# Performance work log

Hardware: AMD Instinct MI355X
Metric: run time of the kernel (lower is better)

The kernel has to match this reference:

```python
import jax, jax.numpy as jnp
import numpy as np

EMBED_DIM = 768
NUM_HEADS = 12
SEGMENT_LENGTHS = (2048, 4096, 8192)
DILATION_RATES = (1, 2, 4)
LN_EPS = 1e-5


def setup_inputs() -> dict:
    rng = jax.random.key(0)
    ks = jax.random.split(rng, 6)
    B, S, E = 2, 8192, EMBED_DIM
    xavier = (2.0 / (E + E)) ** 0.5  # xavier_normal std for square fan-in/out
    return {
        "query": jax.random.normal(ks[0], (B, S, E), jnp.float32),
        "key": jax.random.normal(ks[1], (B, S, E), jnp.float32),
        "value": jax.random.normal(ks[2], (B, S, E), jnp.float32),
        "qkv_w": jax.random.normal(ks[3], (3 * E, E), jnp.float32) * xavier,
        "qkv_b": jnp.zeros((3 * E,), jnp.float32),
        "ln_w": jnp.ones((E,), jnp.float32),
        "ln_b": jnp.zeros((E,), jnp.float32),
        "out_w": jax.random.normal(ks[4], (E, E), jnp.float32) * xavier,
        "out_b": jnp.zeros((E,), jnp.float32),
    }


def _dilated_attention(q, k, v):
    # q,k,v: [b, n, h, d].  Heads are partitioned across the
    # (segment_length, dilation_rate) groups; within each group the sequence
    # is split into segments of length s and subsampled with stride r at
    # offset (i % r); plain softmax attention runs inside each dilated segment.
    b, n, h, d = q.shape
    G = len(SEGMENT_LENGTHS)
    g = h // G
    scale = 1.0 / np.sqrt(d)
    out = jnp.zeros_like(q)
    for i, (s, r) in enumerate(zip(SEGMENT_LENGTHS, DILATION_RATES)):
        off = i % r
        h0, h1 = i * g, (i + 1) * g
        m = n // s
        def seg(x):
            # [b, n, g, d] -> [b, m, s/r, g, d]
            return x[:, :, h0:h1].reshape(b, m, s, g, d)[:, :, off::r]
        qi, ki, vi = seg(q), seg(k), seg(v)
        scores = jnp.einsum("bmqgd,bmkgd->bmgqk", qi, ki) * scale
        p = jax.nn.softmax(scores, axis=-1)
        xi = jnp.einsum("bmgqk,bmkgd->bmqgd", p, vi)
        seg_out = jnp.zeros((b, m, s, g, d), q.dtype).at[:, :, off::r].set(xi)
        out = out.at[:, :, h0:h1].set(seg_out.reshape(b, n, g, d))
    return out / G


def reference(query, key, value, qkv_w, qkv_b, ln_w, ln_b, out_w, out_b):
    B, S, E = query.shape
    H = NUM_HEADS
    d = E // H
    # fused QKV projection (cross-attention path of the fused projection)
    q = (query @ qkv_w[:E].T + qkv_b[:E]).reshape(B, S, H, d)
    k = (key @ qkv_w[E:2 * E].T + qkv_b[E:2 * E]).reshape(B, S, H, d)
    v = (value @ qkv_w[2 * E:].T + qkv_b[2 * E:]).reshape(B, S, H, d)
    x = _dilated_attention(q, k, v).reshape(B, S, E)
    # MAGNETO layer norm before output projection
    mu = jnp.mean(x, axis=-1, keepdims=True)
    var = jnp.mean(jnp.square(x - mu), axis=-1, keepdims=True)
    x = (x - mu) * jax.lax.rsqrt(var + LN_EPS) * ln_w + ln_b
    return x @ out_w.T + out_b
```

## Files before the change

### kernel.cpp

```cpp
#include <hip/hip_runtime.h>
#include <hip/hip_bf16.h>
#include <math.h>

typedef __bf16 bf16_t;
typedef __bf16 bf16x8 __attribute__((ext_vector_type(8)));
typedef __bf16 bf16x4 __attribute__((ext_vector_type(4)));
typedef float f32x4 __attribute__((ext_vector_type(4)));

__device__ __forceinline__ void async_ld16(const void* g, void* l) {
  __builtin_amdgcn_global_load_lds(
      (const __attribute__((address_space(1))) unsigned int*)g,
      (__attribute__((address_space(3))) unsigned int*)l, 16, 0, 0);
}

#define BATCH 2
#define SEQ   8192
#define EMB   768
#define NHEAD 12
#define HD    64
#define TOK   (BATCH*SEQ)
#define GATH_PER_B 57344

__device__ __forceinline__ int headoff(int h) {
  int g = h >> 2;
  int base = (g == 0) ? 0 : ((g == 1) ? 32768 : 49152);
  return base + (h & 3) * (8192 >> g);
}

__global__ void k_cast(const float* __restrict__ in, bf16_t* __restrict__ out, int n) {
  int i = (blockIdx.x * blockDim.x + threadIdx.x) * 8;
  if (i < n) {
    float4 a = *(const float4*)(in + i);
    float4 b = *(const float4*)(in + i + 4);
    __attribute__((aligned(16))) bf16_t o[8] = {
        (bf16_t)a.x, (bf16_t)a.y, (bf16_t)a.z, (bf16_t)a.w,
        (bf16_t)b.x, (bf16_t)b.y, (bf16_t)b.z, (bf16_t)b.w};
    *(uint4*)(out + i) = *(uint4*)o;
  }
}

__global__ __launch_bounds__(256, 2)
void k_gemm_qkv(const bf16_t* __restrict__ qb, const bf16_t* __restrict__ kb,
                const bf16_t* __restrict__ vb, const bf16_t* __restrict__ wqkv,
                const float* __restrict__ qkv_bias,
                bf16_t* __restrict__ Qg, bf16_t* __restrict__ Kg, bf16_t* __restrict__ Vb) {
  const int N = 768, K = 768;
  int z = blockIdx.z;
  const bf16_t* A = (z == 0) ? qb : (z == 1) ? kb : vb;
  const bf16_t* W = wqkv + (size_t)z * N * K;
  const float* bias = qkv_bias + z * N;

  __shared__ bf16_t As[128][32];
  __shared__ bf16_t Bs[128][32];

  int tid = threadIdx.x;
  int wave = tid >> 6, lane = tid & 63;
  int q = lane >> 4, c = lane & 15;
  int wm = (wave & 1) * 64, wn = (wave >> 1) * 64;
  int m0 = blockIdx.y * 128, n0 = blockIdx.x * 128;

  f32x4 acc[4][4];
#pragma unroll
  for (int i = 0; i < 4; i++)
#pragma unroll
    for (int j = 0; j < 4; j++) acc[i][j] = (f32x4){0.f, 0.f, 0.f, 0.f};

  for (int k0 = 0; k0 < K; k0 += 32) {
#pragma unroll
    for (int it = 0; it < 2; ++it) {
      int ch = tid + it * 256;
      int row = ch >> 2, kb8 = (ch & 3) << 3;
      async_ld16(A + (size_t)(m0 + row) * K + k0 + kb8, &As[row][kb8]);
      async_ld16(W + (size_t)(n0 + row) * K + k0 + kb8, &Bs[row][kb8]);
    }
    __syncthreads();
    bf16x8 af[4], bfr[4];
#pragma unroll
    for (int mi = 0; mi < 4; mi++) af[mi] = *(const bf16x8*)&As[wm + mi * 16 + c][q * 8];
#pragma unroll
    for (int nj = 0; nj < 4; nj++) bfr[nj] = *(const bf16x8*)&Bs[wn + nj * 16 + c][q * 8];
#pragma unroll
    for (int mi = 0; mi < 4; mi++)
#pragma unroll
      for (int nj = 0; nj < 4; nj++)
        acc[mi][nj] = __builtin_amdgcn_mfma_f32_16x16x32_bf16(af[mi], bfr[nj], acc[mi][nj], 0, 0, 0);
    __syncthreads();
  }

  if (z == 2) {
#pragma unroll
    for (int mi = 0; mi < 4; mi++)
#pragma unroll
      for (int nj = 0; nj < 4; nj++)
#pragma unroll
        for (int rg = 0; rg < 4; rg++) {
          int row = m0 + wm + mi * 16 + q * 4 + rg;
          int col = n0 + wn + nj * 16 + c;
          Vb[(size_t)row * N + col] = (bf16_t)(acc[mi][nj][rg] + bias[col]);
        }
  } else {
    bf16_t* dst = (z == 0) ? Qg : Kg;
    float qscale = (z == 0) ? 0.125f : 1.0f;
#pragma unroll
    for (int mi = 0; mi < 4; mi++)
#pragma unroll
      for (int nj = 0; nj < 4; nj++) {
        int e = n0 + wn + nj * 16 + c;
        int h = e >> 6, dim = e & 63, g2 = h >> 2;
        int rm1 = (1 << g2) - 1, sh = 11 + g2;
        int smask = (2048 << g2) - 1;
        int ho = headoff(h);
#pragma unroll
        for (int rg = 0; rg < 4; rg++) {
          int row = m0 + wm + mi * 16 + q * 4 + rg;
          float v = (acc[mi][nj][rg] + bias[e]) * qscale;
          int bb = row >> 13, p = row & 8191;
          int t = (p & smask) - g2;
          if (t >= 0 && (t & rm1) == 0) {
            int jj = (p >> sh) * 2048 + (t >> g2);
            dst[(size_t)(bb * GATH_PER_B + ho + jj) * HD + dim] = (bf16_t)v;
          }
        }
      }
  }
}

__global__ __launch_bounds__(256, 2)
void k_gemm_out(const bf16_t* __restrict__ A, const bf16_t* __restrict__ W,
                const float* __restrict__ bias, float* __restrict__ C) {
  const int N = 768, K = 768;
  __shared__ bf16_t As[128][32];
  __shared__ bf16_t Bs[128][32];

  int tid = threadIdx.x;
  int wave = tid >> 6, lane = tid & 63;
  int q = lane >> 4, c = lane & 15;
  int wm = (wave & 1) * 64, wn = (wave >> 1) * 64;
  int m0 = blockIdx.y * 128, n0 = blockIdx.x * 128;

  f32x4 acc[4][4];
#pragma unroll
  for (int i = 0; i < 4; i++)
#pragma unroll
    for (int j = 0; j < 4; j++) acc[i][j] = (f32x4){0.f, 0.f, 0.f, 0.f};

  for (int k0 = 0; k0 < K; k0 += 32) {
#pragma unroll
    for (int it = 0; it < 2; ++it) {
      int ch = tid + it * 256;
      int row = ch >> 2, kb8 = (ch & 3) << 3;
      async_ld16(A + (size_t)(m0 + row) * K + k0 + kb8, &As[row][kb8]);
      async_ld16(W + (size_t)(n0 + row) * K + k0 + kb8, &Bs[row][kb8]);
    }
    __syncthreads();
    bf16x8 af[4], bfr[4];
#pragma unroll
    for (int mi = 0; mi < 4; mi++) af[mi] = *(const bf16x8*)&As[wm + mi * 16 + c][q * 8];
#pragma unroll
    for (int nj = 0; nj < 4; nj++) bfr[nj] = *(const bf16x8*)&Bs[wn + nj * 16 + c][q * 8];
#pragma unroll
    for (int mi = 0; mi < 4; mi++)
#pragma unroll
      for (int nj = 0; nj < 4; nj++)
        acc[mi][nj] = __builtin_amdgcn_mfma_f32_16x16x32_bf16(af[mi], bfr[nj], acc[mi][nj], 0, 0, 0);
    __syncthreads();
  }
#pragma unroll
  for (int mi = 0; mi < 4; mi++)
#pragma unroll
    for (int nj = 0; nj < 4; nj++)
#pragma unroll
      for (int rg = 0; rg < 4; rg++) {
        int row = m0 + wm + mi * 16 + q * 4 + rg;
        int col = n0 + wn + nj * 16 + c;
        C[(size_t)row * N + col] = acc[mi][nj][rg] + bias[col];
      }
}

__global__ __launch_bounds__(256)
void k_gather_v(const bf16_t* __restrict__ Vb, bf16_t* __restrict__ Vt) {
  int h = blockIdx.y, b = blockIdx.z;
  int g = h >> 2;
  int L = 8192 >> g;
  int jj0 = blockIdx.x * 64;
  if (jj0 >= L) return;
  int s = 2048 << g;
  int hb = b * GATH_PER_B + headoff(h);
  int tid = threadIdx.x;

  __shared__ bf16_t tile[64][72];

#pragma unroll
  for (int it = 0; it < 2; ++it) {
    int ch = tid + it * 256;
    int rowl = ch >> 3, db = (ch & 7) << 3;
    int jj = jj0 + rowl;
    int p = (jj >> 11) * s + g + ((jj & 2047) << g);
    *(uint4*)&tile[rowl][db] = *(const uint4*)(Vb + ((size_t)(b * SEQ + p)) * EMB + h * HD + db);
  }
  __syncthreads();
  int dim = tid >> 2, sub = tid & 3;
  __attribute__((aligned(16))) bf16_t tmp[16];
#pragma unroll
  for (int sl = 0; sl < 16; sl++) {
    int t = sub * 16 + sl;
    int pos = (t & 3) * 16 + (t >> 2);
    tmp[sl] = tile[pos][dim];
  }
  size_t vdst = ((size_t)hb) * HD + (size_t)dim * L + jj0 + sub * 16;
  *(uint4*)(Vt + vdst) = *(uint4*)&tmp[0];
  *(uint4*)(Vt + vdst + 8) = *(uint4*)&tmp[8];
}

__global__ __launch_bounds__(256, 3)
void k_attn(const bf16_t* __restrict__ Qg, const bf16_t* __restrict__ Kg,
            const bf16_t* __restrict__ Vt, bf16_t* __restrict__ xattn) {
  int u = blockIdx.x;
  int seg = u % 56, qt = u / 56;
  int b = seg / 28, t = seg % 28;
  int g, h, si;
  if (t < 16)      { g = 0; h = t >> 2;              si = t & 3; }
  else if (t < 24) { g = 1; h = 4 + ((t - 16) >> 1); si = (t - 16) & 1; }
  else             { g = 2; h = 8 + (t - 24);        si = 0; }
  int L = 8192 >> g, s = 2048 << g;
  int hb = b * GATH_PER_B + headoff(h);
  int jj0 = si * 2048 + qt * 128;
  int kvbase = si * 2048;

  __shared__ bf16_t Ps[128][64];
  __shared__ bf16_t Ks[128][64];
  __shared__ bf16_t Vs[64][128];

  int tid = threadIdx.x, wave = tid >> 6, lane = tid & 63;
  int q = lane >> 4, c = lane & 15;
  int cx = c & 7;
  int wm = wave * 32;

  bf16_t* Qs = &Ps[0][0];
#pragma unroll
  for (int it = 0; it < 4; ++it) {
    int ch = tid + it * 256;
    int row = ch >> 3, pc = ch & 7, lc = pc ^ (row & 7);
    async_ld16(Qg + ((size_t)(hb + jj0 + row)) * HD + lc * 8, Qs + ch * 8);
  }
  __syncthreads();
  bf16x8 aq[2][2];
#pragma unroll
  for (int mi = 0; mi < 2; mi++)
#pragma unroll
    for (int kq = 0; kq < 2; kq++) {
      int pch = (kq * 4 + q) ^ cx;
      aq[mi][kq] = *(const bf16x8*)(Qs + (size_t)(wm + mi * 16 + c) * HD + pch * 8);
    }

  float lrow[2][4];
  f32x4 O[2][4];
#pragma unroll
  for (int mi = 0; mi < 2; mi++)
#pragma unroll
    for (int rg = 0; rg < 4; rg++) lrow[mi][rg] = 0.f;
#pragma unroll
  for (int mi = 0; mi < 2; mi++)
#pragma unroll
    for (int vd = 0; vd < 4; vd++) O[mi][vd] = (f32x4){0.f, 0.f, 0.f, 0.f};

  for (int kt = 0; kt < 16; ++kt) {
    __syncthreads();
#pragma unroll
    for (int it = 0; it < 4; ++it) {
      int ch = tid + it * 256;
      int row = ch >> 3, pc = ch & 7, lc = pc ^ (row & 7);
      async_ld16(Kg + ((size_t)(hb + kvbase + kt * 128 + row)) * HD + lc * 8,
                 &Ks[0][0] + ch * 8);
    }
#pragma unroll
    for (int it = 0; it < 4; ++it) {
      int ch = tid + it * 256;
      int dim = ch >> 4, pc = ch & 15, lc = pc ^ (dim & 7);
      async_ld16(Vt + ((size_t)hb) * HD + (size_t)dim * L + kvbase + kt * 128 + lc * 8,
                 &Vs[0][0] + ch * 8);
    }
    __syncthreads();

    f32x4 Sv[2][8];
#pragma unroll
    for (int mi = 0; mi < 2; mi++)
#pragma unroll
      for (int nj = 0; nj < 8; nj++) Sv[mi][nj] = (f32x4){0.f, 0.f, 0.f, 0.f};
#pragma unroll
    for (int kq = 0; kq < 2; kq++) {
      int pch = (kq * 4 + q) ^ cx;
      bf16x8 bk[8];
#pragma unroll
      for (int nj = 0; nj < 8; nj++) bk[nj] = *(const bf16x8*)&Ks[nj * 16 + c][pch * 8];
#pragma unroll
      for (int mi = 0; mi < 2; mi++)
#pragma unroll
        for (int nj = 0; nj < 8; nj++)
          Sv[mi][nj] = __builtin_amdgcn_mfma_f32_16x16x32_bf16(aq[mi][kq], bk[nj], Sv[mi][nj], 0, 0, 0);
    }

#pragma unroll
    for (int half = 0; half < 2; ++half) {
#pragma unroll
      for (int mi = 0; mi < 2; mi++)
#pragma unroll
        for (int rg = 0; rg < 4; rg++) {
          bf16x4 p4;
          float rs = 0.f;
#pragma unroll
          for (int j = 0; j < 4; j++) {
            float p = __expf(Sv[mi][half * 4 + j][rg]);
            rs += p;
            p4[j] = (bf16_t)p;
          }
          lrow[mi][rg] += rs;
          int row = wm + mi * 16 + q * 4 + rg;
          int u8 = c ^ ((row & 7) << 1);
          *(bf16x4*)((char*)&Ps[row][0] + u8 * 8) = p4;
        }
#pragma unroll
      for (int kk2 = 0; kk2 < 2; ++kk2) {
        bf16x8 ap[2], bv[4];
#pragma unroll
        for (int mi = 0; mi < 2; mi++) {
          int u8 = (kk2 * 8 + q * 2) ^ (cx << 1);
          ap[mi] = *(const bf16x8*)((char*)&Ps[wm + mi * 16 + c][0] + u8 * 8);
        }
#pragma unroll
        for (int vd = 0; vd < 4; vd++) {
          int pch = (half * 8 + kk2 * 4 + q) ^ cx;
          bv[vd] = *(const bf16x8*)&Vs[vd * 16 + c][pch * 8];
        }
#pragma unroll
        for (int mi = 0; mi < 2; mi++)
#pragma unroll
          for (int vd = 0; vd < 4; vd++)
            O[mi][vd] = __builtin_amdgcn_mfma_f32_16x16x32_bf16(ap[mi], bv[vd], O[mi][vd], 0, 0, 0);
      }
    }
  }

  const float inv3 = 1.0f / 3.0f;
#pragma unroll
  for (int mi = 0; mi < 2; mi++)
#pragma unroll
    for (int rg = 0; rg < 4; rg++) {
      float l = lrow[mi][rg];
#pragma unroll
      for (int d = 1; d < 16; d <<= 1) l += __shfl_xor(l, d, 64);
      float invl = inv3 / l;
      int jj = jj0 + wm + mi * 16 + q * 4 + rg;
      int p = si * s + g + ((jj & 2047) << g);
      size_t base = ((size_t)(b * SEQ + p)) * EMB + h * HD;
#pragma unroll
      for (int vd = 0; vd < 4; vd++)
        xattn[base + vd * 16 + c] = (bf16_t)(O[mi][vd][rg] * invl);
    }
}

__global__ __launch_bounds__(256)
void k_ln(const bf16_t* __restrict__ x, const float* __restrict__ lnw,
          const float* __restrict__ lnb, bf16_t* __restrict__ y) {
  int wave = threadIdx.x >> 6, lane = threadIdx.x & 63;
  int row = blockIdx.x * 4 + wave;
  const bf16_t* xr = x + (size_t)row * EMB + lane * 12;
  bf16x4 v4[3];
#pragma unroll
  for (int j = 0; j < 3; j++) v4[j] = *(const bf16x4*)(xr + j * 4);
  float v[12], s = 0.f, s2 = 0.f;
#pragma unroll
  for (int j = 0; j < 12; j++) {
    v[j] = (float)v4[j >> 2][j & 3];
    s += v[j];
    s2 += v[j] * v[j];
  }
#pragma unroll
  for (int d = 1; d < 64; d <<= 1) { s += __shfl_xor(s, d, 64); s2 += __shfl_xor(s2, d, 64); }
  float mu = s * (1.f / 768.f);
  float var = s2 * (1.f / 768.f) - mu * mu;
  float rstd = rsqrtf(var + 1e-5f);
  const float4* wr = (const float4*)(lnw + lane * 12);
  const float4* br = (const float4*)(lnb + lane * 12);
  bf16_t* yr = y + (size_t)row * EMB + lane * 12;
#pragma unroll
  for (int j = 0; j < 3; j++) {
    float4 w = wr[j], bb = br[j];
    bf16x4 o;
    o[0] = (bf16_t)((v[j * 4 + 0] - mu) * rstd * w.x + bb.x);
    o[1] = (bf16_t)((v[j * 4 + 1] - mu) * rstd * w.y + bb.y);
    o[2] = (bf16_t)((v[j * 4 + 2] - mu) * rstd * w.z + bb.z);
    o[3] = (bf16_t)((v[j * 4 + 3] - mu) * rstd * w.w + bb.w);
    *(bf16x4*)(yr + j * 4) = o;
  }
}

extern "C" void kernel_launch(void* const* d_in, const int* in_sizes, int n_in,
                              void* d_out, int out_size, void* d_ws, size_t ws_size,
                              hipStream_t stream) {
  const float* query = (const float*)d_in[0];
  const float* key   = (const float*)d_in[1];
  const float* value = (const float*)d_in[2];
  const float* qkv_w = (const float*)d_in[3];
  const float* qkv_b = (const float*)d_in[4];
  const float* ln_w  = (const float*)d_in[5];
  const float* ln_b  = (const float*)d_in[6];
  const float* out_w = (const float*)d_in[7];
  const float* out_b = (const float*)d_in[8];
  float* out = (float*)d_out;

  char* ws = (char*)d_ws;
  const size_t A = (size_t)TOK * EMB * 2;
  bf16_t* qb    = (bf16_t*)(ws + 0 * A);
  bf16_t* kb    = (bf16_t*)(ws + 1 * A);
  bf16_t* vb    = (bf16_t*)(ws + 2 * A);
  bf16_t* Vb    = (bf16_t*)(ws + 3 * A);
  bf16_t* Qg    = (bf16_t*)(ws + 4 * A);
  bf16_t* Kg    = (bf16_t*)(ws + 5 * A);
  bf16_t* wqkv  = (bf16_t*)(ws + 6 * A);
  bf16_t* wout  = (bf16_t*)(ws + 6 * A + (size_t)2304 * 768 * 2);
  bf16_t* Vt    = vb;
  bf16_t* xattn = qb;
  bf16_t* xnorm = kb;

  k_cast<<<6144, 256, 0, stream>>>(query, qb, TOK * EMB);
  k_cast<<<6144, 256, 0, stream>>>(key,   kb, TOK * EMB);
  k_cast<<<6144, 256, 0, stream>>>(value, vb, TOK * EMB);
  k_cast<<<864, 256, 0, stream>>>(qkv_w, wqkv, 2304 * 768);
  k_cast<<<288, 256, 0, stream>>>(out_w, wout, 768 * 768);

  dim3 gq(6, 128, 3);
  k_gemm_qkv<<<gq, 256, 0, stream>>>(qb, kb, vb, wqkv, qkv_b, Qg, Kg, Vb);

  dim3 gg(128, 12, 2);
  k_gather_v<<<gg, 256, 0, stream>>>(Vb, Vt);

  hipMemsetAsync(xattn, 0, A, stream);
  k_attn<<<896, 256, 0, stream>>>(Qg, Kg, Vt, xattn);

  k_ln<<<4096, 256, 0, stream>>>(xattn, ln_w, ln_b, xnorm);

  dim3 go(6, 128);
  k_gemm_out<<<go, 256, 0, stream>>>(xnorm, wout, out_b, out);
}
```

Baseline: 452.0 us.

## Double-buffer LDS tiles in GEMMs and attention, use exp2 with folded log2e

The QKV and output GEMMs and the attention kernel now keep two LDS buffers and issue async loads for the next K/V or A/B tile before computing on the current one. This removes one barrier per iteration and lets global loads overlap MFMA work. The attention softmax switches to a hardware exp2, with log2(e) folded into the Q scale at projection time. The larger LDS footprint lowers the attention launch-bounds occupancy hint from 3 to 2 blocks, so there is less latency hiding from concurrent blocks.

Result: faster. 438.5 us (-3.0%).

```diff
diff --git a/kernel.cpp b/kernel.cpp
--- a/kernel.cpp
+++ b/kernel.cpp
@@ -25,6 +25,14 @@
   int g = h >> 2;
   int base = (g == 0) ? 0 : ((g == 1) ? 32768 : 49152);
   return base + (h & 3) * (8192 >> g);
+}
+
+__device__ __forceinline__ float fast_exp2(float x) {
+#if __has_builtin(__builtin_amdgcn_exp2f)
+  return __builtin_amdgcn_exp2f(x);
+#else
+  return exp2f(x);
+#endif
 }
 
 __global__ void k_cast(const float* __restrict__ in, bf16_t* __restrict__ out, int n) {
@@ -50,8 +58,8 @@
   const bf16_t* W = wqkv + (size_t)z * N * K;
   const float* bias = qkv_bias + z * N;
 
-  __shared__ bf16_t As[128][32];
-  __shared__ bf16_t Bs[128][32];
+  __shared__ bf16_t As[2][128][32];
+  __shared__ bf16_t Bs[2][128][32];
 
   int tid = threadIdx.x;
   int wave = tid >> 6, lane = tid & 63;
@@ -59,32 +67,38 @@
   int wm = (wave & 1) * 64, wn = (wave >> 1) * 64;
   int m0 = blockIdx.y * 128, n0 = blockIdx.x * 128;
 
-  f32x4 acc[4][4];
-#pragma unroll
-  for (int i = 0; i < 4; i++)
-#pragma unroll
-    for (int j = 0; j < 4; j++) acc[i][j] = (f32x4){0.f, 0.f, 0.f, 0.f};
-
-  for (int k0 = 0; k0 < K; k0 += 32) {
+  auto stage = [&](int k0, int bsel) {
 #pragma unroll
     for (int it = 0; it < 2; ++it) {
       int ch = tid + it * 256;
       int row = ch >> 2, kb8 = (ch & 3) << 3;
-      async_ld16(A + (size_t)(m0 + row) * K + k0 + kb8, &As[row][kb8]);
-      async_ld16(W + (size_t)(n0 + row) * K + k0 + kb8, &Bs[row][kb8]);
-    }
+      async_ld16(A + (size_t)(m0 + row) * K + k0 + kb8, &As[bsel][row][kb8]);
+      async_ld16(W + (size_t)(n0 + row) * K + k0 + kb8, &Bs[bsel][row][kb8]);
+    }
+  };
+
+  f32x4 acc[4][4];
+#pragma unroll
+  for (int i = 0; i < 4; i++)
+#pragma unroll
+    for (int j = 0; j < 4; j++) acc[i][j] = (f32x4){0.f, 0.f, 0.f, 0.f};
+
+  stage(0, 0);
+#pragma unroll 2
+  for (int kt = 0; kt < 24; ++kt) {
+    int cur = kt & 1;
     __syncthreads();
+    if (kt + 1 < 24) stage((kt + 1) * 32, cur ^ 1);
     bf16x8 af[4], bfr[4];
 #pragma unroll
-    for (int mi = 0; mi < 4; mi++) af[mi] = *(const bf16x8*)&As[wm + mi * 16 + c][q * 8];
-#pragma unroll
-    for (int nj = 0; nj < 4; nj++) bfr[nj] = *(const bf16x8*)&Bs[wn + nj * 16 + c][q * 8];
+    for (int mi = 0; mi < 4; mi++) af[mi] = *(const bf16x8*)&As[cur][wm + mi * 16 + c][q * 8];
+#pragma unroll
+    for (int nj = 0; nj < 4; nj++) bfr[nj] = *(const bf16x8*)&Bs[cur][wn + nj * 16 + c][q * 8];
 #pragma unroll
     for (int mi = 0; mi < 4; mi++)
 #pragma unroll
       for (int nj = 0; nj < 4; nj++)
         acc[mi][nj] = __builtin_amdgcn_mfma_f32_16x16x32_bf16(af[mi], bfr[nj], acc[mi][nj], 0, 0, 0);
-    __syncthreads();
   }
 
   if (z == 2) {
@@ -100,7 +114,7 @@
         }
   } else {
     bf16_t* dst = (z == 0) ? Qg : Kg;
-    float qscale = (z == 0) ? 0.125f : 1.0f;
+    float qscale = (z == 0) ? 0.125f * 1.44269504088896f : 1.0f;
 #pragma unroll
     for (int mi = 0; mi < 4; mi++)
 #pragma unroll
@@ -129,8 +143,8 @@
 void k_gemm_out(const bf16_t* __restrict__ A, const bf16_t* __restrict__ W,
                 const float* __restrict__ bias, float* __restrict__ C) {
   const int N = 768, K = 768;
-  __shared__ bf16_t As[128][32];
-  __shared__ bf16_t Bs[128][32];
+  __shared__ bf16_t As[2][128][32];
+  __shared__ bf16_t Bs[2][128][32];
 
   int tid = threadIdx.x;
   int wave = tid >> 6, lane = tid & 63;
@@ -138,32 +152,38 @@
   int wm = (wave & 1) * 64, wn = (wave >> 1) * 64;
   int m0 = blockIdx.y * 128, n0 = blockIdx.x * 128;
 
-  f32x4 acc[4][4];
-#pragma unroll
-  for (int i = 0; i < 4; i++)
-#pragma unroll
-    for (int j = 0; j < 4; j++) acc[i][j] = (f32x4){0.f, 0.f, 0.f, 0.f};
-
-  for (int k0 = 0; k0 < K; k0 += 32) {
+  auto stage = [&](int k0, int bsel) {
 #pragma unroll
     for (int it = 0; it < 2; ++it) {
       int ch = tid + it * 256;
       int row = ch >> 2, kb8 = (ch & 3) << 3;
-      async_ld16(A + (size_t)(m0 + row) * K + k0 + kb8, &As[row][kb8]);
-      async_ld16(W + (size_t)(n0 + row) * K + k0 + kb8, &Bs[row][kb8]);
-    }
+      async_ld16(A + (size_t)(m0 + row) * K + k0 + kb8, &As[bsel][row][kb8]);
+      async_ld16(W + (size_t)(n0 + row) * K + k0 + kb8, &Bs[bsel][row][kb8]);
+    }
+  };
+
+  f32x4 acc[4][4];
+#pragma unroll
+  for (int i = 0; i < 4; i++)
+#pragma unroll
+    for (int j = 0; j < 4; j++) acc[i][j] = (f32x4){0.f, 0.f, 0.f, 0.f};
+
+  stage(0, 0);
+#pragma unroll 2
+  for (int kt = 0; kt < 24; ++kt) {
+    int cur = kt & 1;
     __syncthreads();
+    if (kt + 1 < 24) stage((kt + 1) * 32, cur ^ 1);
     bf16x8 af[4], bfr[4];
 #pragma unroll
-    for (int mi = 0; mi < 4; mi++) af[mi] = *(const bf16x8*)&As[wm + mi * 16 + c][q * 8];
-#pragma unroll
-    for (int nj = 0; nj < 4; nj++) bfr[nj] = *(const bf16x8*)&Bs[wn + nj * 16 + c][q * 8];
+    for (int mi = 0; mi < 4; mi++) af[mi] = *(const bf16x8*)&As[cur][wm + mi * 16 + c][q * 8];
+#pragma unroll
+    for (int nj = 0; nj < 4; nj++) bfr[nj] = *(const bf16x8*)&Bs[cur][wn + nj * 16 + c][q * 8];
 #pragma unroll
     for (int mi = 0; mi < 4; mi++)
 #pragma unroll
       for (int nj = 0; nj < 4; nj++)
         acc[mi][nj] = __builtin_amdgcn_mfma_f32_16x16x32_bf16(af[mi], bfr[nj], acc[mi][nj], 0, 0, 0);
-    __syncthreads();
   }
 #pragma unroll
   for (int mi = 0; mi < 4; mi++)
@@ -212,7 +232,7 @@
   *(uint4*)(Vt + vdst + 8) = *(uint4*)&tmp[8];
 }
 
-__global__ __launch_bounds__(256, 3)
+__global__ __launch_bounds__(256, 2)
 void k_attn(const bf16_t* __restrict__ Qg, const bf16_t* __restrict__ Kg,
             const bf16_t* __restrict__ Vt, bf16_t* __restrict__ xattn) {
   int u = blockIdx.x;
@@ -228,14 +248,33 @@
   int kvbase = si * 2048;
 
   __shared__ bf16_t Ps[128][64];
-  __shared__ bf16_t Ks[128][64];
-  __shared__ bf16_t Vs[64][128];
+  __shared__ bf16_t Ks[2][128][64];
+  __shared__ bf16_t Vs[2][64][128];
 
   int tid = threadIdx.x, wave = tid >> 6, lane = tid & 63;
   int q = lane >> 4, c = lane & 15;
   int cx = c & 7;
   int wm = wave * 32;
 
+  auto stageK = [&](int kt, int bsel) {
+#pragma unroll
+    for (int it = 0; it < 4; ++it) {
+      int ch = tid + it * 256;
+      int row = ch >> 3, pc = ch & 7, lc = pc ^ (row & 7);
+      async_ld16(Kg + ((size_t)(hb + kvbase + kt * 128 + row)) * HD + lc * 8,
+                 &Ks[bsel][0][0] + ch * 8);
+    }
+  };
+  auto stageV = [&](int kt, int bsel) {
+#pragma unroll
+    for (int it = 0; it < 4; ++it) {
+      int ch = tid + it * 256;
+      int dim = ch >> 4, pc = ch & 15, lc = pc ^ (dim & 7);
+      async_ld16(Vt + ((size_t)hb) * HD + (size_t)dim * L + kvbase + kt * 128 + lc * 8,
+                 &Vs[bsel][0][0] + ch * 8);
+    }
+  };
+
   bf16_t* Qs = &Ps[0][0];
 #pragma unroll
   for (int it = 0; it < 4; ++it) {
@@ -243,7 +282,10 @@
     int row = ch >> 3, pc = ch & 7, lc = pc ^ (row & 7);
     async_ld16(Qg + ((size_t)(hb + jj0 + row)) * HD + lc * 8, Qs + ch * 8);
   }
+  stageK(0, 0);
+  stageV(0, 0);
   __syncthreads();
+
   bf16x8 aq[2][2];
 #pragma unroll
   for (int mi = 0; mi < 2; mi++)
@@ -264,23 +306,13 @@
 #pragma unroll
     for (int vd = 0; vd < 4; vd++) O[mi][vd] = (f32x4){0.f, 0.f, 0.f, 0.f};
 
+#pragma unroll 2
   for (int kt = 0; kt < 16; ++kt) {
-    __syncthreads();
-#pragma unroll
-    for (int it = 0; it < 4; ++it) {
-      int ch = tid + it * 256;
-      int row = ch >> 3, pc = ch & 7, lc = pc ^ (row & 7);
-      async_ld16(Kg + ((size_t)(hb + kvbase + kt * 128 + row)) * HD + lc * 8,
-                 &Ks[0][0] + ch * 8);
-    }
-#pragma unroll
-    for (int it = 0; it < 4; ++it) {
-      int ch = tid + it * 256;
-      int dim = ch >> 4, pc = ch & 15, lc = pc ^ (dim & 7);
-      async_ld16(Vt + ((size_t)hb) * HD + (size_t)dim * L + kvbase + kt * 128 + lc * 8,
-                 &Vs[0][0] + ch * 8);
-    }
-    __syncthreads();
+    int cur = kt & 1;
+    if (kt < 15) {
+      stageK(kt + 1, cur ^ 1);
+      stageV(kt + 1, cur ^ 1);
+    }
 
     f32x4 Sv[2][8];
 #pragma unroll
@@ -292,7 +324,7 @@
       int pch = (kq * 4 + q) ^ cx;
       bf16x8 bk[8];
 #pragma unroll
-      for (int nj = 0; nj < 8; nj++) bk[nj] = *(const bf16x8*)&Ks[nj * 16 + c][pch * 8];
+      for (int nj = 0; nj < 8; nj++) bk[nj] = *(const bf16x8*)&Ks[cur][nj * 16 + c][pch * 8];
 #pragma unroll
       for (int mi = 0; mi < 2; mi++)
 #pragma unroll
@@ -310,7 +342,7 @@
           float rs = 0.f;
 #pragma unroll
           for (int j = 0; j < 4; j++) {
-            float p = __expf(Sv[mi][half * 4 + j][rg]);
+            float p = fast_exp2(Sv[mi][half * 4 + j][rg]);
             rs += p;
             p4[j] = (bf16_t)p;
           }
@@ -330,7 +362,7 @@
 #pragma unroll
         for (int vd = 0; vd < 4; vd++) {
           int pch = (half * 8 + kk2 * 4 + q) ^ cx;
-          bv[vd] = *(const bf16x8*)&Vs[vd * 16 + c][pch * 8];
+          bv[vd] = *(const bf16x8*)&Vs[cur][vd * 16 + c][pch * 8];
         }
 #pragma unroll
         for (int mi = 0; mi < 2; mi++)
@@ -339,6 +371,7 @@
             O[mi][vd] = __builtin_amdgcn_mfma_f32_16x16x32_bf16(ap[mi], bv[vd], O[mi][vd], 0, 0, 0);
       }
     }
+    __syncthreads();
   }
 
   const float inv3 = 1.0f / 3.0f;
```
